# Optimization experiments

Measured on AMD Instinct MI355X. Metric: run time of the kernel, lower is better.

The kernel has to match this reference:

```python
import jax, jax.numpy as jnp
import numpy as np

N_CODES = 1024
CODE_DIM = 256
DECAY = 0.99
EPS = 1e-05


def setup_inputs() -> dict:
    key = jax.random.key(0)
    k1, k2, k3, k4 = jax.random.split(key, 4)
    z = jax.random.normal(k1, (32, CODE_DIM, 32, 32), dtype=jnp.float32)
    embed = jax.random.normal(k2, (N_CODES, CODE_DIM), dtype=jnp.float32)
    cluster_size = jax.random.uniform(k3, (N_CODES,), dtype=jnp.float32)
    embed_avg = jax.random.normal(k4, (N_CODES, CODE_DIM), dtype=jnp.float32)
    return {"z": z, "embed": embed, "cluster_size": cluster_size, "embed_avg": embed_avg}


def reference(z, embed, cluster_size, embed_avg):
    B, D, H, W = z.shape
    K = embed.shape[0]
    # (B*H*W, D) tokens
    flat = jnp.transpose(z, (0, 2, 3, 1)).reshape(-1, D)
    distances = (
        jnp.sum(flat * flat, axis=1, keepdims=True)
        - 2.0 * flat @ embed.T
        + jnp.sum(embed * embed, axis=1)[None, :]
    )
    indices = jnp.argmin(distances, axis=1)  # (N,)
    z_q = embed[indices].reshape(B, H, W, D).transpose(0, 3, 1, 2)  # (B, D, H, W)

    # EMA codebook update (training mode), no onehot materialization
    cs = jax.ops.segment_sum(jnp.ones(flat.shape[0], dtype=flat.dtype), indices, num_segments=K)
    es = jax.ops.segment_sum(flat, indices, num_segments=K)
    new_cluster_size = cluster_size * DECAY + (1.0 - DECAY) * cs
    new_embed_avg = embed_avg * DECAY + (1.0 - DECAY) * es
    n = jnp.sum(new_cluster_size)
    cs_norm = (new_cluster_size + EPS) / (n + K * EPS) * n
    new_embed = new_embed_avg / cs_norm[:, None]

    # straight-through estimator
    z_q_st = z + jax.lax.stop_gradient(z_q - z)
    # torch: F.mse_loss(z.detach(), z_q) -> grads flow to z_q (codebook) only
    vq_loss = jnp.mean((jax.lax.stop_gradient(z) - z_q) ** 2)
    return (z_q_st, indices.reshape(B, H, W), vq_loss, new_embed, new_cluster_size, new_embed_avg)
```

## Files before the change

kernel.cpp:

```cpp
#include <hip/hip_runtime.h>
#include <stdint.h>

#define DECAY 0.99f
#define OMDECAY 0.01f
#define EPSV 1e-5f


typedef _Float16 half8 __attribute__((ext_vector_type(8)));
typedef float floatx4 __attribute__((ext_vector_type(4)));

typedef __attribute__((address_space(1))) const uint32_t gu32;
typedef __attribute__((address_space(3))) uint32_t lu32;

__device__ __forceinline__ void gld16(uint32_t* l, const uint32_t* g) {
    __builtin_amdgcn_global_load_lds((gu32*)g, (lu32*)l, 16, 0, 0);
}

__device__ __forceinline__ uint32_t pack_hl(float v) {
    _Float16 h = (_Float16)v;
    _Float16 lo = (_Float16)(v - (float)h);
    return (uint32_t)__builtin_bit_cast(unsigned short, h) |
           ((uint32_t)__builtin_bit_cast(unsigned short, lo) << 16);
}

__device__ __forceinline__ unsigned int encf(float s) {
    unsigned int b = __builtin_bit_cast(unsigned int, s);
    return (b & 0x80000000u) ? ~b : (b | 0x80000000u);
}

__global__ void prep_embed(const float* __restrict__ embed,
                           unsigned short* __restrict__ B_hi16,
                           unsigned short* __restrict__ B_lo16,
                           float* __restrict__ enorm,
                           float* __restrict__ cs ,
                           uint32_t* __restrict__ b64i) {
    __shared__ float ws4[4];
    const int k = blockIdx.x;
    const int tid = threadIdx.x;
    const int lane = tid & 63;
    const int wv = tid >> 6;
    int idx = k * 256 + tid;
    float v = embed[idx];
    _Float16 h = (_Float16)v;
    _Float16 lo = (_Float16)(v - (float)h);
    B_hi16[idx] = __builtin_bit_cast(unsigned short, h);
    B_lo16[idx] = __builtin_bit_cast(unsigned short, lo);
    float s = v * v;
    for (int off = 32; off > 0; off >>= 1) s += __shfl_down(s, off);
    if (lane == 0) ws4[wv] = s;
    __syncthreads();
    if (tid == 0) enorm[k] = ws4[0] + ws4[1] + ws4[2] + ws4[3];
    if (k < 256) b64i[k * 256 + tid] = 0xFFFFFFFFu;
    if (k == 0) {
        for (int i = tid; i < 2048; i += 256) cs[i] = 0.f;
    }
}

__global__ void split_z(const float* __restrict__ z,
                        uint32_t* __restrict__ A_hi32,
                        uint32_t* __restrict__ A_lo32) {
    __shared__ uint32_t sp[32 * 258];
    const int lane = threadIdx.x & 63;
    const int wv   = threadIdx.x >> 6;
    const int t0   = blockIdx.x * 32;
    const int b    = t0 >> 10;
    const int hw0  = t0 & 1023;
    const int l32  = lane & 31;
    const int dh   = lane >> 5;

    for (int dp = wv; dp < 128; dp += 4) {
        int dd = dp * 2 + dh;
        float v = z[b * 262144 + dd * 1024 + hw0 + l32];
        sp[l32 * 258 + dd] = pack_hl(v);
    }
    __syncthreads();
    for (int r = wv; r < 32; r += 4) {
#pragma unroll
        for (int h2 = 0; h2 < 2; ++h2) {
            int dpair = h2 * 64 + lane;
            uint32_t u0 = sp[r * 258 + 2 * dpair];
            uint32_t u1 = sp[r * 258 + 2 * dpair + 1];
            A_hi32[(t0 + r) * 128 + dpair] = (u0 & 0xffffu) | (u1 << 16);
            A_lo32[(t0 + r) * 128 + dpair] = (u0 >> 16) | (u1 & 0xffff0000u);
        }
    }
}

__global__ __launch_bounds__(256, 2) void vq_mfma(
    const uint32_t* __restrict__ A_hi32,
    const uint32_t* __restrict__ A_lo32,
    const uint32_t* __restrict__ B_hi32,
    const uint32_t* __restrict__ B_lo32,
    const float* __restrict__ enorm,
    unsigned long long* __restrict__ best64)
{
    __shared__ __align__(16) _Float16 AsH[128 * 32];
    __shared__ __align__(16) _Float16 AsL[128 * 32];
    __shared__ __align__(16) _Float16 BsH[256 * 32];
    __shared__ __align__(16) _Float16 BsL[256 * 32];

    const int lane = threadIdx.x & 63;
    const int w    = threadIdx.x >> 6;
    const int q    = lane >> 4;
    const int c16  = lane & 15;
    const int t0   = (blockIdx.x >> 1) * 128;
    const int cb   = (blockIdx.x & 1) * 512;
    const int lane4 = lane >> 2;
    const int dd8   = (lane & 3) * 8;

    for (int nc = 0; nc < 2; ++nc) {
        floatx4 acc[8][4];
#pragma unroll
        for (int i = 0; i < 8; ++i)
#pragma unroll
            for (int j = 0; j < 4; ++j)
                acc[i][j] = (floatx4){0.f, 0.f, 0.f, 0.f};

        for (int dc = 0; dc < 8; ++dc) {
            const int d0 = dc * 32;
            __syncthreads();
            for (int s = w; s < 48; s += 4) {
                if (s < 16) {
                    int ss = s & 7;
                    const uint32_t* base = (s < 8) ? A_hi32 : A_lo32;
                    uint32_t* dst = (uint32_t*)((s < 8) ? AsH : AsL) + ss * 256;
                    int tok = ss * 16 + lane4;
                    gld16(dst, base + (t0 + tok) * 128 + ((d0 + dd8) >> 1));
                } else {
                    int sb = s - 16;
                    int ss = sb & 15;
                    const uint32_t* base = (sb < 16) ? B_hi32 : B_lo32;
                    uint32_t* dst = (uint32_t*)((sb < 16) ? BsH : BsL) + ss * 256;
                    int code = cb + nc * 256 + ss * 16 + lane4;
                    gld16(dst, base + code * 128 + ((d0 + dd8) >> 1));
                }
            }
            __syncthreads();

            half8 bH[4], bL[4];
#pragma unroll
            for (int j = 0; j < 4; ++j) {
                int off = (w * 64 + j * 16 + c16) * 32 + q * 8;
                bH[j] = *(const half8*)(BsH + off);
                bL[j] = *(const half8*)(BsL + off);
            }
#pragma unroll
            for (int i = 0; i < 8; ++i) {
                int off = (i * 16 + c16) * 32 + q * 8;
                half8 aH = *(const half8*)(AsH + off);
                half8 aL = *(const half8*)(AsL + off);
#pragma unroll
                for (int j = 0; j < 4; ++j) {
                    acc[i][j] = __builtin_amdgcn_mfma_f32_16x16x32_f16(aH, bH[j], acc[i][j], 0, 0, 0);
                    acc[i][j] = __builtin_amdgcn_mfma_f32_16x16x32_f16(aH, bL[j], acc[i][j], 0, 0, 0);
                    acc[i][j] = __builtin_amdgcn_mfma_f32_16x16x32_f16(aL, bH[j], acc[i][j], 0, 0, 0);
                }
            }
        }

        float bestv[32];
        int   besti[32];
#pragma unroll
        for (int s = 0; s < 32; ++s) { bestv[s] = 3.4e38f; besti[s] = 0; }
#pragma unroll
        for (int j = 0; j < 4; ++j) {
            int code = cb + nc * 256 + w * 64 + j * 16 + c16;
            float en = enorm[code];
#pragma unroll
            for (int i = 0; i < 8; ++i)
#pragma unroll
                for (int r = 0; r < 4; ++r) {
                    float sc = en - 2.0f * acc[i][j][r];
                    int slot = i * 4 + r;
                    if (sc < bestv[slot] || (sc == bestv[slot] && code < besti[slot])) {
                        bestv[slot] = sc; besti[slot] = code;
                    }
                }
        }
#pragma unroll
        for (int slot = 0; slot < 32; ++slot) {
            float v = bestv[slot]; int bi = besti[slot];
#pragma unroll
            for (int m = 1; m < 16; m <<= 1) {
                float ov = __shfl_xor(v, m);
                int   oi = __shfl_xor(bi, m);
                if (ov < v || (ov == v && oi < bi)) { v = ov; bi = oi; }
            }
            bestv[slot] = v; besti[slot] = bi;
        }
#pragma unroll
        for (int slot = 0; slot < 32; ++slot) {
            if (c16 == (slot & 15)) {
                int tok = (slot >> 2) * 16 + q * 4 + (slot & 3);
                unsigned long long key =
                    ((unsigned long long)encf(bestv[slot]) << 32) |
                    (unsigned int)besti[slot];
                atomicMin(&best64[t0 + tok], key);
            }
        }
    }
}

__global__ __launch_bounds__(256) void merge_zq(
    const unsigned long long* __restrict__ best64,
    const float* __restrict__ z,
    const float* __restrict__ embed,
    float* __restrict__ out_zq,
    float* __restrict__ out_idx,
    float* __restrict__ cs,
    float* __restrict__ loss_sum)
{
    __shared__ int sidx[128];
    const int tid = threadIdx.x;
    const int lane = tid & 63;
    const int w = tid >> 6;
    const int t0 = blockIdx.x * 128;

    if (tid < 128) {
        int bi = (int)(unsigned int)(best64[t0 + tid] & 0xffffffffULL);
        sidx[tid] = bi;
        out_idx[t0 + tid] = (float)bi;
        atomicAdd(&cs[bi], 1.0f);
    }
    __syncthreads();

    const int b_idx = t0 >> 10;
    const int hw0   = t0 & 1023;
    const int zbase = b_idx * 262144 + hw0;
    const int ka = sidx[lane];
    const int kb = sidx[lane + 64];
    float lsum = 0.f;
    for (int d = w; d < 256; d += 4) {
        float zv0 = z[zbase + d * 1024 + lane];
        float zv1 = z[zbase + d * 1024 + lane + 64];
        float e0 = embed[ka * 256 + d];
        float e1 = embed[kb * 256 + d];
        out_zq[zbase + d * 1024 + lane]      = zv0 + (e0 - zv0);
        out_zq[zbase + d * 1024 + lane + 64] = zv1 + (e1 - zv1);
        float d0f = zv0 - e0, d1f = zv1 - e1;
        lsum += d0f * d0f + d1f * d1f;
    }
    for (int off = 32; off > 0; off >>= 1) lsum += __shfl_down(lsum, off);
    if (lane == 0) atomicAdd(loss_sum, lsum);
}

__global__ void vq_finalize_small(const float* __restrict__ cluster_size,
                                  const float* __restrict__ cs,
                                  const float* __restrict__ loss_sum,
                                  float* __restrict__ out_loss,
                                  float* __restrict__ out_ncs,
                                  float* __restrict__ csnorm,
                                  int* __restrict__ offsets,
                                  int* __restrict__ cursor)
{
    __shared__ float wsum[16];
    __shared__ float wncs[16];
    __shared__ float stot[1];
    const int k = threadIdx.x;
    const int lane = k & 63;
    const int wv = k >> 6;
    float cnt = cs[k];
    float ncs = cluster_size[k] * DECAY + OMDECAY * cnt;
    out_ncs[k] = ncs;
    float sc = cnt;
#pragma unroll
    for (int d = 1; d < 64; d <<= 1) {
        float up = __shfl_up(sc, d);
        if (lane >= d) sc += up;
    }
    if (lane == 63) wsum[wv] = sc;
    float ns = ncs;
    for (int off = 32; off > 0; off >>= 1) ns += __shfl_down(ns, off);
    if (lane == 0) wncs[wv] = ns;
    __syncthreads();
    if (wv == 0) {
        float v = (lane < 16) ? wsum[lane] : 0.f;
#pragma unroll
        for (int d = 1; d < 16; d <<= 1) {
            float up = __shfl_up(v, d);
            if (lane >= d) v += up;
        }
        if (lane < 16) wsum[lane] = v;
    } else if (wv == 1) {
        float t = (lane < 16) ? wncs[lane] : 0.f;
        for (int off = 32; off > 0; off >>= 1) t += __shfl_down(t, off);
        if (lane == 0) stot[0] = t;
    }
    __syncthreads();
    float incl = sc + (wv ? wsum[wv - 1] : 0.f);
    int excl = __float2int_rn(incl - cnt);
    offsets[k] = excl;
    cursor[k]  = excl;
    float n = stot[0];
    csnorm[k] = (ncs + EPSV) / (n + 1024.0f * EPSV) * n;
    if (k == 0) out_loss[0] = loss_sum[0] / 8388608.0f;
}

__global__ void scatter_perm(const float* __restrict__ out_idx,
                             int* __restrict__ cursor,
                             int* __restrict__ perm,
                             float* __restrict__ es)
{
    int t = blockIdx.x * 256 + threadIdx.x;
#pragma unroll
    for (int i = 0; i < 8; ++i) es[t + i * 32768] = 0.f;
    int code = (int)out_idx[t];
    int pos = atomicAdd(&cursor[code], 1);
    perm[pos] = t;
}

__global__ void es_sum(const uint32_t* __restrict__ A_hi32,
                       const uint32_t* __restrict__ A_lo32,
                       const int* __restrict__ perm,
                       const float* __restrict__ out_idx,
                       float* __restrict__ es)
{
    __shared__ int sperm[32];
    __shared__ int scode[32];
    const int base = blockIdx.x * 32;
    const int tid = threadIdx.x;
    const int j = tid & 127;
    const uint32_t* __restrict__ A = (tid >> 7) ? A_lo32 : A_hi32;
    if (tid < 32) {
        int t = perm[base + tid];
        sperm[tid] = t;
        scode[tid] = (int)out_idx[t];
    }
    __syncthreads();

    float s0 = 0.f, s1 = 0.f;
    int cur = scode[0];
    uint32_t pu[2];
    pu[0] = A[sperm[0] * 128 + j];
    pu[1] = A[sperm[1] * 128 + j];
#pragma unroll
    for (int i = 0; i < 32; ++i) {
        uint32_t u = pu[i & 1];
        if (i + 2 < 32) pu[i & 1] = A[sperm[i + 2] * 128 + j];
        int code = scode[i];
        if (code != cur) {
            atomicAdd(&es[cur * 256 + 2 * j],     s0);
            atomicAdd(&es[cur * 256 + 2 * j + 1], s1);
            s0 = 0.f; s1 = 0.f; cur = code;
        }
        s0 += (float)__builtin_bit_cast(_Float16, (unsigned short)(u & 0xffffu));
        s1 += (float)__builtin_bit_cast(_Float16, (unsigned short)(u >> 16));
    }
    atomicAdd(&es[cur * 256 + 2 * j],     s0);
    atomicAdd(&es[cur * 256 + 2 * j + 1], s1);
}

__global__ void finalize_embed(const float* __restrict__ embed_avg,
                               const float* __restrict__ es,
                               const float* __restrict__ csnorm,
                               float* __restrict__ out_embed,
                               float* __restrict__ out_nea)
{
    int idx = blockIdx.x * 256 + threadIdx.x;
    int k = idx >> 8;
    float nea = embed_avg[idx] * DECAY + OMDECAY * es[idx];
    out_nea[idx] = nea;
    out_embed[idx] = nea / csnorm[k];
}

extern "C" void kernel_launch(void* const* d_in, const int* in_sizes, int n_in,
                              void* d_out, int out_size, void* d_ws, size_t ws_size,
                              hipStream_t stream) {
    const float* z            = (const float*)d_in[0];
    const float* embed        = (const float*)d_in[1];
    const float* cluster_size = (const float*)d_in[2];
    const float* embed_avg    = (const float*)d_in[3];
    float* out = (float*)d_out;
    uint32_t* ws32 = (uint32_t*)d_ws;

    uint32_t* B_hi32 = ws32 + 0;
    uint32_t* B_lo32 = ws32 + 131072;
    uint32_t* A_hi32 = ws32 + 262144;
    uint32_t* A_lo32 = ws32 + 4456448;
    int* perm        = (int*)(ws32 + 8650752);
    int* offsets     = (int*)(ws32 + 8683520);
    int* cursor      = (int*)(ws32 + 8684544);
    float* cs        = (float*)(ws32 + 8912896);
    float* loss_sum  = (float*)(ws32 + 8913920);
    float* enorm     = (float*)(ws32 + 8914944);
    float* csnorm    = (float*)(ws32 + 8915968);
    float* es        = (float*)(ws32 + 0);
    unsigned long long* best64 = (unsigned long long*)(out + 8421378);

    prep_embed<<<1024, 256, 0, stream>>>(embed, (unsigned short*)B_hi32,
                                         (unsigned short*)B_lo32, enorm, cs,
                                         (uint32_t*)best64);
    split_z<<<1024, 256, 0, stream>>>(z, A_hi32, A_lo32);
    vq_mfma<<<512, 256, 0, stream>>>(A_hi32, A_lo32, B_hi32, B_lo32, enorm, best64);
    merge_zq<<<256, 256, 0, stream>>>(best64, z, embed,
                                      out, out + 8388608, cs, loss_sum);
    vq_finalize_small<<<1, 1024, 0, stream>>>(cluster_size, cs, loss_sum,
                                              out + 8421376, out + 8683521, csnorm,
                                              offsets, cursor);
    scatter_perm<<<128, 256, 0, stream>>>(out + 8388608, cursor, perm, es);
    es_sum<<<1024, 256, 0, stream>>>(A_hi32, A_lo32, perm, out + 8388608, es);
    finalize_embed<<<1024, 256, 0, stream>>>(embed_avg, es, csnorm,
                                             out + 8421377, out + 8684545);
}
```

Baseline: 264.4 us.

## Double-buffer codebook tiles in LDS and read token fragments directly from global

Codebook (B) tiles now go into two LDS buffers, and the next tile is staged with async global-to-LDS loads while the current one feeds the MFMAs. This leaves one barrier per step instead of two. The token (A) fragments skip LDS and are loaded straight from global memory into registers, which frees LDS for the second B buffer. The cost is that repeated A loads across codebook chunks now depend on L1/L2 hits, and that global-load latency sits directly in the MFMA loop.

```diff
diff --git a/kernel.cpp b/kernel.cpp
--- a/kernel.cpp
+++ b/kernel.cpp
@@ -94,10 +94,8 @@
     const float* __restrict__ enorm,
     unsigned long long* __restrict__ best64)
 {
-    __shared__ __align__(16) _Float16 AsH[128 * 32];
-    __shared__ __align__(16) _Float16 AsL[128 * 32];
-    __shared__ __align__(16) _Float16 BsH[256 * 32];
-    __shared__ __align__(16) _Float16 BsL[256 * 32];
+    __shared__ __align__(16) _Float16 BsH[2][256 * 32];
+    __shared__ __align__(16) _Float16 BsL[2][256 * 32];
 
     const int lane = threadIdx.x & 63;
     const int w    = threadIdx.x >> 6;
@@ -108,6 +106,29 @@
     const int lane4 = lane >> 2;
     const int dd8   = (lane & 3) * 8;
 
+    const uint32_t* aH0 = A_hi32 + (t0 + c16) * 128 + q * 4;
+    const uint32_t* aL0 = A_lo32 + (t0 + c16) * 128 + q * 4;
+
+    auto stageB = [&](int step) {
+        const int nc_s = step >> 3;
+        const int dc_s = step & 7;
+        const int d0h  = (dc_s * 32 + dd8) >> 1;
+        _Float16* dH = BsH[step & 1];
+        _Float16* dL = BsL[step & 1];
+        for (int s = w; s < 32; s += 4) {
+            int ss = s & 15;
+            int code = cb + nc_s * 256 + ss * 16 + lane4;
+            if (s < 16) {
+                gld16((uint32_t*)dH + ss * 256, B_hi32 + code * 128 + d0h);
+            } else {
+                gld16((uint32_t*)dL + ss * 256, B_lo32 + code * 128 + d0h);
+            }
+        }
+    };
+
+    stageB(0);
+    __syncthreads();
+
     for (int nc = 0; nc < 2; ++nc) {
         floatx4 acc[8][4];
 #pragma unroll
@@ -117,38 +138,22 @@
                 acc[i][j] = (floatx4){0.f, 0.f, 0.f, 0.f};
 
         for (int dc = 0; dc < 8; ++dc) {
-            const int d0 = dc * 32;
-            __syncthreads();
-            for (int s = w; s < 48; s += 4) {
-                if (s < 16) {
-                    int ss = s & 7;
-                    const uint32_t* base = (s < 8) ? A_hi32 : A_lo32;
-                    uint32_t* dst = (uint32_t*)((s < 8) ? AsH : AsL) + ss * 256;
-                    int tok = ss * 16 + lane4;
-                    gld16(dst, base + (t0 + tok) * 128 + ((d0 + dd8) >> 1));
-                } else {
-                    int sb = s - 16;
-                    int ss = sb & 15;
-                    const uint32_t* base = (sb < 16) ? B_hi32 : B_lo32;
-                    uint32_t* dst = (uint32_t*)((sb < 16) ? BsH : BsL) + ss * 256;
-                    int code = cb + nc * 256 + ss * 16 + lane4;
-                    gld16(dst, base + code * 128 + ((d0 + dd8) >> 1));
-                }
-            }
-            __syncthreads();
-
+            const int step = nc * 8 + dc;
+            if (step + 1 < 16) stageB(step + 1);
+
+            const _Float16* bsh = BsH[step & 1];
+            const _Float16* bsl = BsL[step & 1];
             half8 bH[4], bL[4];
 #pragma unroll
             for (int j = 0; j < 4; ++j) {
                 int off = (w * 64 + j * 16 + c16) * 32 + q * 8;
-                bH[j] = *(const half8*)(BsH + off);
-                bL[j] = *(const half8*)(BsL + off);
+                bH[j] = *(const half8*)(bsh + off);
+                bL[j] = *(const half8*)(bsl + off);
             }
 #pragma unroll
             for (int i = 0; i < 8; ++i) {
-                int off = (i * 16 + c16) * 32 + q * 8;
-                half8 aH = *(const half8*)(AsH + off);
-                half8 aL = *(const half8*)(AsL + off);
+                half8 aH = *(const half8*)(aH0 + i * 2048 + dc * 16);
+                half8 aL = *(const half8*)(aL0 + i * 2048 + dc * 16);
 #pragma unroll
                 for (int j = 0; j < 4; ++j) {
                     acc[i][j] = __builtin_amdgcn_mfma_f32_16x16x32_f16(aH, bH[j], acc[i][j], 0, 0, 0);
@@ -156,6 +161,7 @@
                     acc[i][j] = __builtin_amdgcn_mfma_f32_16x16x32_f16(aL, bH[j], acc[i][j], 0, 0, 0);
                 }
             }
+            __syncthreads();
         }
 
         float bestv[32];
```

Measured after the change: 293.9 us. 1.11x slower.
